# Kernel tuning notes

Hardware: AMD Instinct MI355X
Metric: run time of the kernel (lower is better)

Reference implementation:

```python
import jax, jax.numpy as jnp
import numpy as np

NUM_HEADS = 16
GRID_SIZE = 16


def rotate(x, pos):
    # x: [B, nH, N, D] with D even; pos: [N] float
    D = x.shape[-1]
    half = D // 2
    omega = jnp.arange(half, dtype=x.dtype) / half
    omega = 1.0 / (10000.0 ** omega)
    freq = pos[:, None].astype(x.dtype) * omega          # [N, half]
    # torch .repeat(1,1,1,2) TILES the last dim (not interleave)
    emb_sin = jnp.tile(jnp.sin(freq), (1, 2))            # [N, D]
    emb_cos = jnp.tile(jnp.cos(freq), (1, 2))
    y = x.reshape(x.shape[:-1] + (half, 2))
    rot = jnp.stack((-y[..., 1], y[..., 0]), axis=-1).reshape(x.shape)
    return x * emb_cos + rot * emb_sin


def setup_inputs() -> dict:
    key = jax.random.key(0)
    k1, k2, k3, k4 = jax.random.split(key, 4)
    B, N, C = 2, 2048, 1024
    return {
        "x": jax.random.normal(k1, (B, N, C), dtype=jnp.float32),
        "W_qkv": jax.random.normal(k2, (3 * C, C), dtype=jnp.float32) * 0.02,
        "W_proj": jax.random.normal(k3, (C, C), dtype=jnp.float32) * 0.02,
        "b_proj": jax.random.normal(k4, (C,), dtype=jnp.float32) * 0.02,
        "T": 8,
        "H": 16,
        "W": 16,
    }


def reference(x, W_qkv, W_proj, b_proj, T, H, W):
    B, N, C = x.shape
    nH = NUM_HEADS
    hd = C // nH
    d_dim = 2 * (hd // 3 // 2)   # 20 for hd=64
    h_dim = d_dim
    w_dim = d_dim

    # axial positions (mask=None path): ids = arange(T*H*W)
    ids = jnp.arange(T * H * W)
    d_pos = (ids // (H * W)).astype(jnp.float32)
    rem = ids % (H * W)
    h_pos = (rem // W).astype(jnp.float32) * (GRID_SIZE / H)
    w_pos = (rem % W).astype(jnp.float32) * (GRID_SIZE / W)

    # fused QKV projection (no bias)
    qkv = jnp.einsum('bnc,oc->bno', x, W_qkv)            # [B, N, 3C]
    qkv = qkv.reshape(B, N, 3, nH, hd).transpose(2, 0, 3, 1, 4)
    q, k, v = qkv[0], qkv[1], qkv[2]                     # [B, nH, N, hd]

    s0, s1, s2 = 0, d_dim, d_dim + h_dim
    s3 = s2 + w_dim
    qd = rotate(q[..., s0:s1], d_pos); kd = rotate(k[..., s0:s1], d_pos)
    qh = rotate(q[..., s1:s2], h_pos); kh = rotate(k[..., s1:s2], h_pos)
    qw = rotate(q[..., s2:s3], w_pos); kw = rotate(k[..., s2:s3], w_pos)
    if s3 < hd:
        q = jnp.concatenate([qd, qh, qw, q[..., s3:]], axis=-1)
        k = jnp.concatenate([kd, kh, kw, k[..., s3:]], axis=-1)
    else:
        q = jnp.concatenate([qd, qh, qw], axis=-1)
        k = jnp.concatenate([kd, kh, kw], axis=-1)

    # SDPA (default scale = hd**-0.5, no dropout, not causal)
    scale = hd ** (-0.5)
    scores = jnp.einsum('bhqd,bhkd->bhqk', q, k) * scale
    attn = jax.nn.softmax(scores, axis=-1)
    out = jnp.einsum('bhqk,bhkd->bhqd', attn, v)          # [B, nH, N, hd]

    out = out.transpose(0, 2, 1, 3).reshape(B, N, C)
    out = jnp.einsum('bnc,oc->bno', out, W_proj) + b_proj
    return out


if __name__ == "__main__":
    inp = setup_inputs()
    y = reference(**inp)
    print(y.shape, y.dtype)
```

## Files before the change

### kernel.cpp

```cpp
#include <hip/hip_runtime.h>
#include <stdint.h>

typedef unsigned short u16;
typedef __attribute__((ext_vector_type(8))) short bf16x8;
typedef __attribute__((ext_vector_type(4))) float f32x4;
typedef __attribute__((ext_vector_type(16))) float f32x16;
typedef __attribute__((ext_vector_type(2))) unsigned int u32x2;

#define DEVI static __device__ __forceinline__

static constexpr int NTOK = 2048;
static constexpr int CDIM = 1024;
static constexpr int C3   = 3072;

DEVI u16 f2bf(float f) {
  uint32_t u = __float_as_uint(f);
  return (u16)((u + 0x7fffu + ((u >> 16) & 1u)) >> 16);
}

DEVI float exp2fast(float x) { return __builtin_amdgcn_exp2f(x); }

DEVI void gl_lds16(const void* g, void* l) {
  __builtin_amdgcn_global_load_lds(
      (__attribute__((address_space(1))) uint32_t*)g,
      (__attribute__((address_space(3))) uint32_t*)l, 16, 0, 0);
}

DEVI f32x4 mfma16(bf16x8 a, bf16x8 b, f32x4 c) {
  return __builtin_amdgcn_mfma_f32_16x16x32_bf16(a, b, c, 0, 0, 0);
}
DEVI f32x16 mfma32(bf16x8 a, bf16x8 b, f32x16 c) {
  return __builtin_amdgcn_mfma_f32_32x32x16_bf16(a, b, c, 0, 0, 0);
}

__global__ void k_cvt3(const float* __restrict__ x, const float* __restrict__ wq,
                       const float* __restrict__ wp, u16* __restrict__ xb,
                       u16* __restrict__ wqb, u16* __restrict__ wpb) {
  int i = (blockIdx.x * blockDim.x + threadIdx.x) * 4;
  const float* src; u16* dst; int off;
  if (i < 4194304)      { src = x;  dst = xb;  off = i; }
  else if (i < 7340032) { src = wq; dst = wqb; off = i - 4194304; }
  else                  { src = wp; dst = wpb; off = i - 7340032; }
  float4 v = *reinterpret_cast<const float4*>(src + off);
  ushort4 o;
  o.x = f2bf(v.x); o.y = f2bf(v.y); o.z = f2bf(v.z); o.w = f2bf(v.w);
  *reinterpret_cast<ushort4*>(dst + off) = o;
}

template<int MODE>
__global__ __launch_bounds__(256, 2) void k_gemm(
    const u16* __restrict__ A, const u16* __restrict__ Bw,
    float* __restrict__ Cout, const float* __restrict__ bias,
    u16* __restrict__ qb, u16* __restrict__ kb, u16* __restrict__ vT,
    int Nn, int K) {
  constexpr int NJ = (MODE == 1) ? 2 : 4;
  constexpr int WN = NJ * 16;
  __shared__ u16 smem[MODE == 2 ? 17408 : 6144];
  u16* Al = smem;
  u16* Bl = smem + 4096;
  const int tid = threadIdx.x, wid = tid >> 6, lane = tid & 63;
  const int bm = blockIdx.x, bn = blockIdx.y;
  const int wr = wid >> 1, wc = wid & 1;
  const int fr = lane & 15, fg = lane >> 4;
  f32x4 acc[4][NJ] = {};

  const int r0 = wid * 16 + (lane >> 2);
  const int c0 = (lane & 3) * 8;
  const u16* Ag = A + (size_t)(bm * 128) * K + c0;
  const u16* Bg = Bw + (size_t)(bn * (MODE == 1 ? 64 : 128)) * K + c0;
  u16* Alb = Al + wid * 512;
  u16* Blb = Bl + wid * 512;
  const int fk = fg * 8;

  for (int kt = 0; kt < K; kt += 32) {
    __syncthreads();
    gl_lds16(Ag + (size_t)r0 * K + kt,        Alb);
    gl_lds16(Ag + (size_t)(64 + r0) * K + kt, Alb + 2048);
    gl_lds16(Bg + (size_t)r0 * K + kt,        Blb);
    if constexpr (MODE == 2)
      gl_lds16(Bg + (size_t)(64 + r0) * K + kt, Blb + 2048);
    __syncthreads();
    bf16x8 af[4], bfr[NJ];
#pragma unroll
    for (int i = 0; i < 4; ++i)
      af[i] = *reinterpret_cast<const bf16x8*>(&Al[(wr * 64 + i * 16 + fr) * 32 + fk]);
#pragma unroll
    for (int j = 0; j < NJ; ++j)
      bfr[j] = *reinterpret_cast<const bf16x8*>(&Bl[(wc * WN + j * 16 + fr) * 32 + fk]);
#pragma unroll
    for (int i = 0; i < 4; ++i)
#pragma unroll
      for (int j = 0; j < NJ; ++j)
        acc[i][j] = mfma16(af[i], bfr[j], acc[i][j]);
  }
  const int orow0 = bm * 128 + wr * 64 + fg * 4;

  if constexpr (MODE == 1) {
    const int ocol0 = bn * 64 + wc * 32 + fr;
#pragma unroll
    for (int j = 0; j < NJ; ++j) {
      int col = ocol0 + j * 16;
      float badd = bias[col];
#pragma unroll
      for (int i = 0; i < 4; ++i)
#pragma unroll
        for (int r = 0; r < 4; ++r)
          Cout[(size_t)(orow0 + i * 16 + r) * Nn + col] = acc[i][j][r] + badd;
    }
  } else {
    const int which = bn >> 3;
    if (which < 2) {
      const int cbase = (bn & 7) * 128 + wc * 64 + fr;
      u16* dst = (which == 0) ? qb : kb;
#pragma unroll
      for (int j = 0; j < 4; ++j) {
        const int c = cbase + j * 16;
        const int d = c & 63, hh = c >> 6;
        const bool dorope = (d < 60);
        int seg = 0; float omega = 0.f;
        if (dorope) {
          seg = d / 20;
          int ds = d - seg * 20;
          int jj = (ds >= 10) ? ds - 10 : ds;
          omega = exp2fast(-1.3287712379549449f * (float)jj);
        }
#pragma unroll
        for (int i = 0; i < 4; ++i) {
#pragma unroll
          for (int r = 0; r < 4; ++r) {
            const int m = orow0 + i * 16 + r;
            const int b = m >> 11, n = m & (NTOK - 1);
            float val = acc[i][j][r];
            float pr = __shfl_xor(val, 1, 64);
            float outv = val;
            if (dorope) {
              float pos = (seg == 0) ? (float)(n >> 8)
                        : (seg == 1) ? (float)((n >> 4) & 15)
                                     : (float)(n & 15);
              float f = pos * omega, sn, cs;
              __sincosf(f, &sn, &cs);
              outv = (d & 1) ? val * cs + pr * sn : val * cs - pr * sn;
            }
            if (which == 0) outv *= 0.18033688011112042f;
            dst[((size_t)(b * 16 + hh) * NTOK + n) * 64 + d] = f2bf(outv);
          }
        }
      }
    } else {
      __syncthreads();
      const int mbase = wr * 64 + fg * 4;
#pragma unroll
      for (int j = 0; j < 4; ++j) {
        const int crow = wc * 64 + j * 16 + fr;
#pragma unroll
        for (int i = 0; i < 4; ++i) {
          ushort4 pk;
          pk.x = f2bf(acc[i][j][0]); pk.y = f2bf(acc[i][j][1]);
          pk.z = f2bf(acc[i][j][2]); pk.w = f2bf(acc[i][j][3]);
          *reinterpret_cast<ushort4*>(&smem[crow * 136 + mbase + i * 16]) = pk;
        }
      }
      __syncthreads();
      const int c = tid >> 1, mh = (tid & 1) * 64;
      const int cfull = (bn & 7) * 128 + c;
      const int hh = cfull >> 6, d = cfull & 63;
      const int b = bm >> 4;
      u16* dst = vT + (((size_t)(b * 16 + hh)) * 64 + d) * NTOK + (bm & 15) * 128 + mh;
      const u16* srcl = &smem[c * 136 + mh];
#pragma unroll
      for (int s = 0; s < 8; ++s)
        *reinterpret_cast<bf16x8*>(dst + s * 8) = *reinterpret_cast<const bf16x8*>(srcl + s * 8);
    }
  }
}

__global__ __launch_bounds__(256, 2) void k_attn(
    const u16* __restrict__ qp, const u16* __restrict__ kp,
    const u16* __restrict__ vp, u16* __restrict__ op) {
  __shared__ u16 Kl[2][64 * 64];
  __shared__ u16 Vl[2][64 * 64];
  const int bh = blockIdx.x;
  const int qt = blockIdx.y;
  const int tid = threadIdx.x, wid = tid >> 6, lane = tid & 63;
  const int lo = lane & 31, hi = lane >> 5;

  int koff[4];
#pragma unroll
  for (int c = 0; c < 4; ++c) koff[c] = (((c * 2 + hi) ^ (lo & 7)) * 8);
  const int lbase = lo * 64;

  const int q0 = qt * 128 + wid * 32;
  const u16* qrow = qp + ((size_t)bh * NTOK + q0 + lo) * 64 + hi * 8;
  bf16x8 qf[4];
#pragma unroll
  for (int c = 0; c < 4; ++c)
    qf[c] = *reinterpret_cast<const bf16x8*>(qrow + c * 16);

  f32x16 acc2[2] = {};
  float lrun = 0.f;

  const int srow = lane >> 3;
  const int scol = ((lane & 7) ^ srow) * 8;
  const u16* kg = kp + ((size_t)bh * NTOK + wid * 8 + srow) * 64 + scol;
  const u16* vg = vp + ((size_t)bh * 64 + wid * 8 + srow) * NTOK + scol;

  auto stage = [&](int buf, int kvt) {
#pragma unroll
    for (int s = 0; s < 2; ++s) {
      gl_lds16(kg + (size_t)(kvt + s * 32) * 64, &Kl[buf][s * 2048 + wid * 512]);
      gl_lds16(vg + (size_t)(s * 32) * NTOK + kvt, &Vl[buf][s * 2048 + wid * 512]);
    }
  };

  stage(0, 0);
  __syncthreads();
  int cur = 0;
  for (int kvt = 0; kvt < NTOK; kvt += 64) {
    if (kvt + 64 < NTOK) stage(cur ^ 1, kvt + 64);
    const u16* Kc = &Kl[cur][0];
    const u16* Vc = &Vl[cur][0];
    float ps = 0.f;

#pragma unroll
    for (int mt = 0; mt < 2; ++mt) {
      f32x16 s = {};
      const u16* Kh = Kc + mt * 2048 + lbase;
      __builtin_amdgcn_s_setprio(1);
#pragma unroll
      for (int c = 0; c < 4; ++c) {
        bf16x8 kf = *reinterpret_cast<const bf16x8*>(Kh + koff[c]);
        s = mfma32(kf, qf[c], s);
      }
      __builtin_amdgcn_s_setprio(0);

      uint32_t pk[8];
#pragma unroll
      for (int jj = 0; jj < 8; ++jj) {
        float p0 = exp2fast(s[2 * jj]);
        float p1 = exp2fast(s[2 * jj + 1]);
        ps += p0 + p1;
        uint32_t w;
        asm("v_cvt_pk_bf16_f32 %0, %1, %2" : "=v"(w) : "v"(p0), "v"(p1));
        pk[jj] = w;
      }
      bf16x8 pa[2];
#pragma unroll
      for (int ksl = 0; ksl < 2; ++ksl) {
        const int g = ksl * 4;
        u32x2 sA = __builtin_amdgcn_permlane32_swap(pk[g + 0], pk[g + 2], false, false);
        u32x2 sB = __builtin_amdgcn_permlane32_swap(pk[g + 1], pk[g + 3], false, false);
        union { uint32_t u[4]; bf16x8 v; } x;
        x.u[0] = sA[0]; x.u[1] = sB[0]; x.u[2] = sA[1]; x.u[3] = sB[1];
        pa[ksl] = x.v;
      }

      __builtin_amdgcn_s_setprio(1);
#pragma unroll
      for (int nf = 0; nf < 2; ++nf) {
        const u16* Vh = Vc + nf * 2048 + lbase;
#pragma unroll
        for (int ksl = 0; ksl < 2; ++ksl) {
          bf16x8 vf = *reinterpret_cast<const bf16x8*>(Vh + koff[mt * 2 + ksl]);
          acc2[nf] = mfma32(pa[ksl], vf, acc2[nf]);
        }
      }
      __builtin_amdgcn_s_setprio(0);
    }

    ps += __shfl_xor(ps, 32, 64);
    lrun += ps;
    __syncthreads();
    cur ^= 1;
  }

  const int b = bh >> 4, h = bh & 15;
  float linv[16];
#pragma unroll
  for (int r = 0; r < 16; ++r)
    linv[r] = 1.f / __shfl(lrun, (r & 3) + 8 * (r >> 2) + 4 * hi, 64);
#pragma unroll
  for (int nf = 0; nf < 2; ++nf)
#pragma unroll
    for (int r = 0; r < 16; ++r) {
      int n = q0 + (r & 3) + 8 * (r >> 2) + 4 * hi;
      int col = h * 64 + nf * 32 + lo;
      op[((size_t)b * NTOK + n) * CDIM + col] = f2bf(acc2[nf][r] * linv[r]);
    }
}

extern "C" void kernel_launch(void* const* d_in, const int* in_sizes, int n_in,
                              void* d_out, int out_size, void* d_ws, size_t ws_size,
                              hipStream_t stream) {
  (void)in_sizes; (void)n_in; (void)out_size; (void)ws_size;
  const float* x  = (const float*)d_in[0];
  const float* Wq = (const float*)d_in[1];
  const float* Wp = (const float*)d_in[2];
  const float* bp = (const float*)d_in[3];

  char* w = (char*)d_ws;
  u16* x_bf  = (u16*)(w + 0);
  u16* wq_bf = (u16*)(w + 8388608);
  u16* wp_bf = (u16*)(w + 14680064);
  u16* q_bf  = (u16*)(w + 16777216);
  u16* k_bf  = (u16*)(w + 25165824);
  u16* vT    = (u16*)(w + 33554432);
  u16* at_bf = (u16*)(w + 41943040);

  k_cvt3<<<8192, 256, 0, stream>>>(x, Wq, Wp, x_bf, wq_bf, wp_bf);

  k_gemm<2><<<dim3(32, 24), 256, 0, stream>>>(x_bf, wq_bf, nullptr, nullptr,
                                              q_bf, k_bf, vT, C3, CDIM);

  k_attn<<<dim3(32, 16), 256, 0, stream>>>(q_bf, k_bf, vT, at_bf);

  k_gemm<1><<<dim3(32, 16), 256, 0, stream>>>(at_bf, wp_bf, (float*)d_out, bp,
                                              nullptr, nullptr, nullptr, CDIM, CDIM);
}
```

Measured before the change: 115.5 us.

## Process two 32-row query sub-tiles per warp in attention to reuse K/V fragments

Each warp in the attention kernel now handles 64 query rows (two 32-row sub-tiles) instead of 32, so every K and V fragment read from LDS feeds two MFMAs. The query tile per block doubles to 256 and the grid halves to 32x8. Launch bounds drop to one block per SM to allow the extra accumulator and Q registers. The aim is fewer LDS reads and less staging per unit of work, at the cost of more register pressure, lower occupancy and fewer blocks (256) to spread across the CUs.

```diff
diff --git a/kernel.cpp b/kernel.cpp
--- a/kernel.cpp
+++ b/kernel.cpp
@@ -174,7 +174,7 @@
   }
 }
 
-__global__ __launch_bounds__(256, 2) void k_attn(
+__global__ __launch_bounds__(256, 1) void k_attn(
     const u16* __restrict__ qp, const u16* __restrict__ kp,
     const u16* __restrict__ vp, u16* __restrict__ op) {
   __shared__ u16 Kl[2][64 * 64];
@@ -189,15 +189,18 @@
   for (int c = 0; c < 4; ++c) koff[c] = (((c * 2 + hi) ^ (lo & 7)) * 8);
   const int lbase = lo * 64;
 
-  const int q0 = qt * 128 + wid * 32;
-  const u16* qrow = qp + ((size_t)bh * NTOK + q0 + lo) * 64 + hi * 8;
-  bf16x8 qf[4];
-#pragma unroll
-  for (int c = 0; c < 4; ++c)
-    qf[c] = *reinterpret_cast<const bf16x8*>(qrow + c * 16);
-
-  f32x16 acc2[2] = {};
-  float lrun = 0.f;
+  const int q0 = qt * 256 + wid * 64;
+  bf16x8 qf[2][4];
+#pragma unroll
+  for (int qa = 0; qa < 2; ++qa) {
+    const u16* qrow = qp + ((size_t)bh * NTOK + q0 + qa * 32 + lo) * 64 + hi * 8;
+#pragma unroll
+    for (int c = 0; c < 4; ++c)
+      qf[qa][c] = *reinterpret_cast<const bf16x8*>(qrow + c * 16);
+  }
+
+  f32x16 acc2[2][2] = {};
+  float lrun[2] = {0.f, 0.f};
 
   const int srow = lane >> 3;
   const int scol = ((lane & 7) ^ srow) * 8;
@@ -219,39 +222,44 @@
     if (kvt + 64 < NTOK) stage(cur ^ 1, kvt + 64);
     const u16* Kc = &Kl[cur][0];
     const u16* Vc = &Vl[cur][0];
-    float ps = 0.f;
+    float ps[2] = {0.f, 0.f};
 
 #pragma unroll
     for (int mt = 0; mt < 2; ++mt) {
-      f32x16 s = {};
       const u16* Kh = Kc + mt * 2048 + lbase;
-      __builtin_amdgcn_s_setprio(1);
-#pragma unroll
-      for (int c = 0; c < 4; ++c) {
-        bf16x8 kf = *reinterpret_cast<const bf16x8*>(Kh + koff[c]);
-        s = mfma32(kf, qf[c], s);
-      }
-      __builtin_amdgcn_s_setprio(0);
-
-      uint32_t pk[8];
-#pragma unroll
-      for (int jj = 0; jj < 8; ++jj) {
-        float p0 = exp2fast(s[2 * jj]);
-        float p1 = exp2fast(s[2 * jj + 1]);
-        ps += p0 + p1;
-        uint32_t w;
-        asm("v_cvt_pk_bf16_f32 %0, %1, %2" : "=v"(w) : "v"(p0), "v"(p1));
-        pk[jj] = w;
-      }
-      bf16x8 pa[2];
-#pragma unroll
-      for (int ksl = 0; ksl < 2; ++ksl) {
-        const int g = ksl * 4;
-        u32x2 sA = __builtin_amdgcn_permlane32_swap(pk[g + 0], pk[g + 2], false, false);
-        u32x2 sB = __builtin_amdgcn_permlane32_swap(pk[g + 1], pk[g + 3], false, false);
-        union { uint32_t u[4]; bf16x8 v; } x;
-        x.u[0] = sA[0]; x.u[1] = sB[0]; x.u[2] = sA[1]; x.u[3] = sB[1];
-        pa[ksl] = x.v;
+      bf16x8 kf[4];
+#pragma unroll
+      for (int c = 0; c < 4; ++c)
+        kf[c] = *reinterpret_cast<const bf16x8*>(Kh + koff[c]);
+
+      bf16x8 pa[2][2];
+#pragma unroll
+      for (int qa = 0; qa < 2; ++qa) {
+        f32x16 s = {};
+        __builtin_amdgcn_s_setprio(1);
+#pragma unroll
+        for (int c = 0; c < 4; ++c) s = mfma32(kf[c], qf[qa][c], s);
+        __builtin_amdgcn_s_setprio(0);
+
+        uint32_t pk[8];
+#pragma unroll
+        for (int jj = 0; jj < 8; ++jj) {
+          float p0 = exp2fast(s[2 * jj]);
+          float p1 = exp2fast(s[2 * jj + 1]);
+          ps[qa] += p0 + p1;
+          uint32_t w;
+          asm("v_cvt_pk_bf16_f32 %0, %1, %2" : "=v"(w) : "v"(p0), "v"(p1));
+          pk[jj] = w;
+        }
+#pragma unroll
+        for (int ksl = 0; ksl < 2; ++ksl) {
+          const int g = ksl * 4;
+          u32x2 sA = __builtin_amdgcn_permlane32_swap(pk[g + 0], pk[g + 2], false, false);
+          u32x2 sB = __builtin_amdgcn_permlane32_swap(pk[g + 1], pk[g + 3], false, false);
+          union { uint32_t u[4]; bf16x8 v; } x;
+          x.u[0] = sA[0]; x.u[1] = sB[0]; x.u[2] = sA[1]; x.u[3] = sB[1];
+          pa[qa][ksl] = x.v;
+        }
       }
 
       __builtin_amdgcn_s_setprio(1);
@@ -261,31 +269,39 @@
 #pragma unroll
         for (int ksl = 0; ksl < 2; ++ksl) {
           bf16x8 vf = *reinterpret_cast<const bf16x8*>(Vh + koff[mt * 2 + ksl]);
-          acc2[nf] = mfma32(pa[ksl], vf, acc2[nf]);
+          acc2[0][nf] = mfma32(pa[0][ksl], vf, acc2[0][nf]);
+          acc2[1][nf] = mfma32(pa[1][ksl], vf, acc2[1][nf]);
         }
       }
       __builtin_amdgcn_s_setprio(0);
     }
 
-    ps += __shfl_xor(ps, 32, 64);
-    lrun += ps;
+#pragma unroll
+    for (int qa = 0; qa < 2; ++qa) {
+      float p = ps[qa];
+      p += __shfl_xor(p, 32, 64);
+      lrun[qa] += p;
+    }
     __syncthreads();
     cur ^= 1;
   }
 
   const int b = bh >> 4, h = bh & 15;
-  float linv[16];
-#pragma unroll
-  for (int r = 0; r < 16; ++r)
-    linv[r] = 1.f / __shfl(lrun, (r & 3) + 8 * (r >> 2) + 4 * hi, 64);
-#pragma unroll
-  for (int nf = 0; nf < 2; ++nf)
-#pragma unroll
-    for (int r = 0; r < 16; ++r) {
-      int n = q0 + (r & 3) + 8 * (r >> 2) + 4 * hi;
-      int col = h * 64 + nf * 32 + lo;
-      op[((size_t)b * NTOK + n) * CDIM + col] = f2bf(acc2[nf][r] * linv[r]);
-    }
+#pragma unroll
+  for (int qa = 0; qa < 2; ++qa) {
+    float linv[16];
+#pragma unroll
+    for (int r = 0; r < 16; ++r)
+      linv[r] = 1.f / __shfl(lrun[qa], (r & 3) + 8 * (r >> 2) + 4 * hi, 64);
+#pragma unroll
+    for (int nf = 0; nf < 2; ++nf)
+#pragma unroll
+      for (int r = 0; r < 16; ++r) {
+        int n = q0 + qa * 32 + (r & 3) + 8 * (r >> 2) + 4 * hi;
+        int col = h * 64 + nf * 32 + lo;
+        op[((size_t)b * NTOK + n) * CDIM + col] = f2bf(acc2[qa][nf][r] * linv[r]);
+      }
+  }
 }
 
 extern "C" void kernel_launch(void* const* d_in, const int* in_sizes, int n_in,
@@ -311,7 +327,7 @@
   k_gemm<2><<<dim3(32, 24), 256, 0, stream>>>(x_bf, wq_bf, nullptr, nullptr,
                                               q_bf, k_bf, vT, C3, CDIM);
 
-  k_attn<<<dim3(32, 16), 256, 0, stream>>>(q_bf, k_bf, vT, at_bf);
+  k_attn<<<dim3(32, 8), 256, 0, stream>>>(q_bf, k_bf, vT, at_bf);
 
   k_gemm<1><<<dim3(32, 16), 256, 0, stream>>>(at_bf, wp_bf, (float*)d_out, bp,
                                               nullptr, nullptr, nullptr, CDIM, CDIM);
```

Result: slower. 128.1 us (+10.9%).

## Load K and V fragments directly from global memory in attention kernel

Applied to the files above, without the earlier changes.

The attention kernel no longer stages K and V tiles into double-buffered shared memory with async global-to-LDS loads and block barriers. Each wave now reads its MFMA operand fragments for K and V straight from global memory, relying on the cache since the four waves share the same K/V rows. This removes LDS traffic and the per-iteration __syncthreads, but duplicates global loads across waves and loses the prefetch overlap, so latency may be exposed.

```diff
diff --git a/kernel.cpp b/kernel.cpp
--- a/kernel.cpp
+++ b/kernel.cpp
@@ -177,18 +177,11 @@
 __global__ __launch_bounds__(256, 2) void k_attn(
     const u16* __restrict__ qp, const u16* __restrict__ kp,
     const u16* __restrict__ vp, u16* __restrict__ op) {
-  __shared__ u16 Kl[2][64 * 64];
-  __shared__ u16 Vl[2][64 * 64];
   const int bh = blockIdx.x;
   const int qt = blockIdx.y;
   const int tid = threadIdx.x, wid = tid >> 6, lane = tid & 63;
   const int lo = lane & 31, hi = lane >> 5;
 
-  int koff[4];
-#pragma unroll
-  for (int c = 0; c < 4; ++c) koff[c] = (((c * 2 + hi) ^ (lo & 7)) * 8);
-  const int lbase = lo * 64;
-
   const int q0 = qt * 128 + wid * 32;
   const u16* qrow = qp + ((size_t)bh * NTOK + q0 + lo) * 64 + hi * 8;
   bf16x8 qf[4];
@@ -199,36 +192,20 @@
   f32x16 acc2[2] = {};
   float lrun = 0.f;
 
-  const int srow = lane >> 3;
-  const int scol = ((lane & 7) ^ srow) * 8;
-  const u16* kg = kp + ((size_t)bh * NTOK + wid * 8 + srow) * 64 + scol;
-  const u16* vg = vp + ((size_t)bh * 64 + wid * 8 + srow) * NTOK + scol;
-
-  auto stage = [&](int buf, int kvt) {
-#pragma unroll
-    for (int s = 0; s < 2; ++s) {
-      gl_lds16(kg + (size_t)(kvt + s * 32) * 64, &Kl[buf][s * 2048 + wid * 512]);
-      gl_lds16(vg + (size_t)(s * 32) * NTOK + kvt, &Vl[buf][s * 2048 + wid * 512]);
-    }
-  };
-
-  stage(0, 0);
-  __syncthreads();
-  int cur = 0;
+  const u16* kb  = kp + ((size_t)bh * NTOK + lo) * 64 + hi * 8;
+  const u16* vb0 = vp + ((size_t)bh * 64 + lo) * NTOK + hi * 8;
+  const u16* vb1 = vb0 + (size_t)32 * NTOK;
+
   for (int kvt = 0; kvt < NTOK; kvt += 64) {
-    if (kvt + 64 < NTOK) stage(cur ^ 1, kvt + 64);
-    const u16* Kc = &Kl[cur][0];
-    const u16* Vc = &Vl[cur][0];
     float ps = 0.f;
-
 #pragma unroll
     for (int mt = 0; mt < 2; ++mt) {
+      const u16* Kh = kb + (size_t)(kvt + mt * 32) * 64;
       f32x16 s = {};
-      const u16* Kh = Kc + mt * 2048 + lbase;
       __builtin_amdgcn_s_setprio(1);
 #pragma unroll
       for (int c = 0; c < 4; ++c) {
-        bf16x8 kf = *reinterpret_cast<const bf16x8*>(Kh + koff[c]);
+        bf16x8 kf = *reinterpret_cast<const bf16x8*>(Kh + c * 16);
         s = mfma32(kf, qf[c], s);
       }
       __builtin_amdgcn_s_setprio(0);
@@ -257,10 +234,10 @@
       __builtin_amdgcn_s_setprio(1);
 #pragma unroll
       for (int nf = 0; nf < 2; ++nf) {
-        const u16* Vh = Vc + nf * 2048 + lbase;
+        const u16* Vh = (nf ? vb1 : vb0) + kvt + mt * 32;
 #pragma unroll
         for (int ksl = 0; ksl < 2; ++ksl) {
-          bf16x8 vf = *reinterpret_cast<const bf16x8*>(Vh + koff[mt * 2 + ksl]);
+          bf16x8 vf = *reinterpret_cast<const bf16x8*>(Vh + ksl * 16);
           acc2[nf] = mfma32(pa[ksl], vf, acc2[nf]);
         }
       }
@@ -269,8 +246,6 @@
 
     ps += __shfl_xor(ps, 32, 64);
     lrun += ps;
-    __syncthreads();
-    cur ^= 1;
   }
 
   const int b = bh >> 4, h = bh & 15;
```

Result: slower. 187.6 us (+62.4%).
